# Kernel tuning notes

Hardware: AMD Instinct MI355X
Metric: run time of the kernel (lower is better)

The kernel has to match this reference:

```python
import jax, jax.numpy as jnp
import numpy as np

N_NODES = 512   # hidden_dim in the original code == number of graph nodes
SEQ = 64
DIN = 128
HEADS = 4
DOUT = 128
E = 4096
NEG_SLOPE = 0.2
LN_EPS = 1e-5


def _init(key, shape, fan_in):
    return (jax.random.normal(key, shape, jnp.float32) / np.sqrt(fan_in)).astype(jnp.float32)


def setup_inputs() -> dict:
    key = jax.random.key(0)
    ks = jax.random.split(key, 16)
    x = jax.random.normal(ks[0], (N_NODES, SEQ, DIN), jnp.float32)
    src = jax.random.randint(ks[1], (E,), 0, N_NODES, dtype=jnp.int32)
    # guarantee every node has >=1 incoming edge (DGL requires nonzero in-degree)
    dst = jnp.concatenate([
        jnp.arange(N_NODES, dtype=jnp.int32),
        jax.random.randint(ks[2], (E - N_NODES,), 0, N_NODES, dtype=jnp.int32),
    ])
    return {
        "x": x, "src": src, "dst": dst,
        # GATv2 layer 0: DIN -> DIN, 4 heads (separate fc_src / fc_dst, share_weights=False)
        "W1s": _init(ks[3], (DIN, HEADS * DIN), DIN), "b1s": jnp.zeros((HEADS * DIN,), jnp.float32),
        "W1d": _init(ks[4], (DIN, HEADS * DIN), DIN), "b1d": jnp.zeros((HEADS * DIN,), jnp.float32),
        "attn1": _init(ks[5], (HEADS, DIN), DIN),
        # GATv2 layer 1: DIN*HEADS -> DIN, 1 head
        "W2s": _init(ks[6], (HEADS * DIN, DIN), HEADS * DIN), "b2s": jnp.zeros((DIN,), jnp.float32),
        "W2d": _init(ks[7], (HEADS * DIN, DIN), HEADS * DIN), "b2d": jnp.zeros((DIN,), jnp.float32),
        "attn2": _init(ks[8], (1, DIN), DIN),
        # LayerNorm ln0 + final Linear fc
        "gamma": jnp.ones((DIN,), jnp.float32), "beta": jnp.zeros((DIN,), jnp.float32),
        "Wfc": _init(ks[9], (DIN, DOUT), DIN), "bfc": jnp.zeros((DOUT,), jnp.float32),
    }


def _gatv2(h, src, dst, Ws, bs, Wd, bd, attn, n_nodes, heads, d_out):
    """DGL GATv2Conv: h [N, Din] -> [N, heads, d_out]."""
    fs = (h @ Ws + bs).reshape(-1, heads, d_out)   # [N,H,D]
    fd = (h @ Wd + bd).reshape(-1, heads, d_out)
    e = jax.nn.leaky_relu(fs[src] + fd[dst], NEG_SLOPE)     # [E,H,D]
    logits = jnp.einsum('ehd,hd->eh', e, attn)              # [E,H]
    m = jax.ops.segment_max(logits, dst, num_segments=n_nodes)
    ex = jnp.exp(logits - m[dst])
    den = jax.ops.segment_sum(ex, dst, num_segments=n_nodes)
    alpha = ex / den[dst]                                   # edge softmax per dst node
    return jax.ops.segment_sum(alpha[:, :, None] * fs[src], dst, num_segments=n_nodes)


def reference(x, src, dst, W1s, b1s, W1d, b1d, attn1, W2s, b2s, W2d, b2d, attn2, gamma, beta, Wfc, bfc):
    # preprocess: keep channel 0, log10(rest + 1), NaN -> 0
    xp = jnp.concatenate([x[..., :1], jnp.log10(x[..., 1:] + 1.0)], axis=-1)
    xp = jnp.where(jnp.isnan(xp), 0.0, xp)                  # [N, S, DIN]
    h = jnp.transpose(xp, (1, 0, 2))                        # [S, N, DIN] (seq-batched graph copies)
    g1 = jax.vmap(lambda hh: _gatv2(hh, src, dst, W1s, b1s, W1d, b1d, attn1, N_NODES, HEADS, DIN))(h)
    h2 = g1.reshape(SEQ, N_NODES, HEADS * DIN)              # concat heads
    g2 = jax.vmap(lambda hh: _gatv2(hh, src, dst, W2s, b2s, W2d, b2d, attn2, N_NODES, 1, DIN))(h2)
    g = jnp.transpose(g2[:, :, 0, :], (1, 0, 2))            # [N, S, DIN]
    g = jnp.where(jnp.isnan(g), xp, g)
    out = xp + g                                            # residual; dropout is identity in eval
    mu = jnp.mean(out, axis=-1, keepdims=True)
    var = jnp.mean(jnp.square(out - mu), axis=-1, keepdims=True)
    y = (out - mu) / jnp.sqrt(var + LN_EPS) * gamma + beta  # ln0
    return y @ Wfc + bfc                                    # [N, S, DOUT]
```

## Files before the change

kernel.cpp:

```cpp
#include <hip/hip_runtime.h>
#include <cmath>

#define NN    512
#define SEQL  64
#define DIN   128
#define NH    4
#define NE    4096
#define DOUTN 128

typedef __attribute__((ext_vector_type(4))) float f32x4;
typedef __attribute__((ext_vector_type(8))) short bf16x8;

__device__ __forceinline__ float lrelu(float v) { return v >= 0.f ? v : 0.2f * v; }

__device__ __forceinline__ unsigned short f2bf(float f) {
    union { float f; unsigned u; } x; x.f = f;
    unsigned r = (x.u + 0x7FFFu + ((x.u >> 16) & 1u)) >> 16;
    return (unsigned short)r;
}
__device__ __forceinline__ float bf2f(unsigned short h) {
    union { unsigned u; float f; } x; x.u = ((unsigned)h) << 16;
    return x.f;
}

__global__ __launch_bounds__(256) void preprocess_k(const float* __restrict__ x,
                                                    float* __restrict__ H,
                                                    unsigned short* __restrict__ Hbf) {
    int tid = blockIdx.x * 256 + threadIdx.x;
    int base = tid * 4;
    int d0 = base & 127;
    int s  = (base >> 7) & 63;
    int n  = base >> 13;
    float4 v = *(const float4*)(x + base);
    if (d0 == 0) {
        v.y = log10f(v.y + 1.f); v.z = log10f(v.z + 1.f); v.w = log10f(v.w + 1.f);
    } else {
        v.x = log10f(v.x + 1.f); v.y = log10f(v.y + 1.f);
        v.z = log10f(v.z + 1.f); v.w = log10f(v.w + 1.f);
    }
    if (v.x != v.x) v.x = 0.f;
    if (v.y != v.y) v.y = 0.f;
    if (v.z != v.z) v.z = 0.f;
    if (v.w != v.w) v.w = 0.f;
    size_t off = ((size_t)s * NN + n) * DIN + d0;
    *(float4*)(H + off) = v;
    ushort4 b; b.x = f2bf(v.x); b.y = f2bf(v.y); b.z = f2bf(v.z); b.w = f2bf(v.w);
    *(ushort4*)(Hbf + off) = b;
}

__global__ __launch_bounds__(256) void castw_k(const float* __restrict__ W1s, const float* __restrict__ W1d,
                                               const float* __restrict__ W2s, const float* __restrict__ W2d,
                                               const float* __restrict__ Wfc,
                                               const float* __restrict__ b1s, const float* __restrict__ b1d,
                                               const float* __restrict__ b2s, const float* __restrict__ b2d,
                                               unsigned short* __restrict__ T1sd, unsigned short* __restrict__ T2sd,
                                               unsigned short* __restrict__ Tfc,
                                               float* __restrict__ bc1, float* __restrict__ bc2) {
    int i = blockIdx.x * 256 + threadIdx.x;
    if (i < 131072) {
        int n = i >> 7, k = i & 127;
        T1sd[i] = f2bf(n < 512 ? W1s[k * 512 + n] : W1d[k * 512 + (n - 512)]);
    } else if (i < 262144) {
        int j = i - 131072; int n = j >> 9, k = j & 511;
        T2sd[j] = f2bf(n < 128 ? W2s[k * 128 + n] : W2d[k * 128 + (n - 128)]);
    } else if (i < 278528) {
        int j = i - 262144; int n = j >> 7, k = j & 127;
        Tfc[j] = f2bf(Wfc[k * 128 + n]);
    } else if (i < 279552) {
        int j = i - 278528;
        bc1[j] = j < 512 ? b1s[j] : b1d[j - 512];
    } else if (i < 279808) {
        int j = i - 279552;
        bc2[j] = j < 128 ? b2s[j] : b2d[j - 128];
    }
}

__global__ void csr_init_k(int* counts, int* fill) {
    int t = threadIdx.x;
    counts[t] = 0; fill[t] = 0;
}
__global__ void csr_hist_k(const int* __restrict__ dst, int* counts) {
    int e = blockIdx.x * 256 + threadIdx.x;
    if (e < NE) atomicAdd(&counts[dst[e]], 1);
}
__global__ void csr_scan_k(const int* __restrict__ counts, int* __restrict__ row_ptr) {
    int l = threadIdx.x;
    int c[8]; int lsum = 0;
#pragma unroll
    for (int j = 0; j < 8; ++j) { c[j] = counts[l * 8 + j]; lsum += c[j]; }
    int pre = lsum;
    for (int o = 1; o < 64; o <<= 1) {
        int v = __shfl_up(pre, o);
        if (l >= o) pre += v;
    }
    int acc = pre - lsum;
#pragma unroll
    for (int j = 0; j < 8; ++j) { row_ptr[l * 8 + j] = acc; acc += c[j]; }
    if (l == 63) row_ptr[512] = acc;
}
__global__ void csr_scatter_k(const int* __restrict__ dst, const int* __restrict__ row_ptr,
                              int* fill, int* eidx) {
    int e = blockIdx.x * 256 + threadIdx.x;
    if (e < NE) {
        int dn = dst[e];
        int pos = atomicAdd(&fill[dn], 1);
        eidx[row_ptr[dn] + pos] = e;
    }
}

template<int MODE>
__global__ __launch_bounds__(256) void gemm_k(const unsigned short* __restrict__ A,
                                              const unsigned short* __restrict__ BT,
                                              const float* __restrict__ bias,
                                              void* __restrict__ C1v, void* __restrict__ C2v,
                                              int M, int N, int K, int s0, int half) {
    __shared__ unsigned short As[8192];
    __shared__ unsigned short Bs[8192];
    int t = threadIdx.x;
    int w = t >> 6, l = t & 63;
    int wr = w >> 1, wc = w & 1;
    int m0 = blockIdx.y * 128, n0 = blockIdx.x * 128;

    f32x4 acc[4][4];
#pragma unroll
    for (int i = 0; i < 4; ++i)
#pragma unroll
        for (int j = 0; j < 4; ++j) acc[i][j] = (f32x4){0.f, 0.f, 0.f, 0.f};

    for (int k0 = 0; k0 < K; k0 += 64) {
        bf16x8 ra[4], rb[4];
#pragma unroll
        for (int r = 0; r < 4; ++r) {
            int q = t * 16 + r * 4096;
            int row = q >> 7;
            int cole = (q & 127) >> 1;
            ra[r] = *(const bf16x8*)(A  + (size_t)(m0 + row) * K + k0 + cole);
            rb[r] = *(const bf16x8*)(BT + (size_t)(n0 + row) * K + k0 + cole);
        }
        __syncthreads();
#pragma unroll
        for (int r = 0; r < 4; ++r) {
            int q = t * 16 + r * 4096;
            int row = q >> 7;
            int phys = (row << 7) | ((q & 127) ^ ((row & 7) << 4));
            *(bf16x8*)((char*)As + phys) = ra[r];
            *(bf16x8*)((char*)Bs + phys) = rb[r];
        }
        __syncthreads();
#pragma unroll
        for (int ks = 0; ks < 2; ++ks) {
            bf16x8 af[4], bfr[4];
#pragma unroll
            for (int i = 0; i < 4; ++i) {
                int row = wr * 64 + i * 16 + (l & 15);
                int colb = (ks * 64 + ((l >> 4) * 16)) ^ ((row & 7) << 4);
                af[i] = *(const bf16x8*)((const char*)As + (row << 7) + colb);
            }
#pragma unroll
            for (int j = 0; j < 4; ++j) {
                int row = wc * 64 + j * 16 + (l & 15);
                int colb = (ks * 64 + ((l >> 4) * 16)) ^ ((row & 7) << 4);
                bfr[j] = *(const bf16x8*)((const char*)Bs + (row << 7) + colb);
            }
#pragma unroll
            for (int i = 0; i < 4; ++i)
#pragma unroll
                for (int j = 0; j < 4; ++j)
                    acc[i][j] = __builtin_amdgcn_mfma_f32_16x16x32_bf16(af[i], bfr[j], acc[i][j], 0, 0, 0);
        }
    }

    float bl[4];
#pragma unroll
    for (int j = 0; j < 4; ++j) bl[j] = bias[n0 + wc * 64 + j * 16 + (l & 15)];
#pragma unroll
    for (int i = 0; i < 4; ++i) {
#pragma unroll
        for (int j = 0; j < 4; ++j) {
            int n = n0 + wc * 64 + j * 16 + (l & 15);
#pragma unroll
            for (int jj = 0; jj < 4; ++jj) {
                int m = m0 + wr * 64 + i * 16 + (l >> 4) * 4 + jj;
                float v = acc[i][j][jj] + bl[j];
                if (MODE == 1) {
                    int sl = m >> 9, node = m & 511;
                    ((float*)C1v)[((size_t)node * SEQL + (s0 + sl)) * DOUTN + n] = v;
                } else if (MODE == 2) {
                    unsigned short* dp = (unsigned short*)(n < half ? C1v : C2v);
                    int nn = n < half ? n : n - half;
                    dp[(size_t)m * half + nn] = f2bf(v);
                } else {
                    ((unsigned short*)C1v)[(size_t)m * N + n] = f2bf(v);
                }
            }
        }
    }
}

__device__ __forceinline__ void s_swizzle(int bid, int sc, int B, int logB, int& s, int& idx) {
    if ((sc & 7) == 0) {
        int xcd = bid & 7;
        int j = bid >> 3;
        int grp = j >> logB;
        idx = j & (B - 1);
        s = grp * 8 + xcd;
    } else {
        s = bid >> logB;
        idx = bid & (B - 1);
    }
}

__global__ __launch_bounds__(256) void fused_l1_k(const unsigned short* __restrict__ FS,
                                                  const unsigned short* __restrict__ FD,
                                                  const int* __restrict__ src,
                                                  const int* __restrict__ row_ptr,
                                                  const int* __restrict__ eidx,
                                                  const float* __restrict__ attn,
                                                  unsigned short* __restrict__ G1,
                                                  int sc) {
    int wv = threadIdx.x >> 6, l = threadIdx.x & 63;
    int s, nb;
    s_swizzle(blockIdx.x, sc, 128, 7, s, nb);
    int n = nb * 4 + wv;
    int e0 = row_ptr[n], e1 = row_ptr[n + 1];
    float at[8], fdv[8];
    bf16x8 fdr = *(const bf16x8*)(FD + ((size_t)s * NN + n) * 512 + l * 8);
#pragma unroll
    for (int k = 0; k < 8; ++k) { at[k] = attn[l * 8 + k]; fdv[k] = bf2f((unsigned short)fdr[k]); }
    const unsigned short* fsbase = FS + (size_t)s * NN * 512 + l * 8;
    float m_run = -INFINITY, den = 0.f;
    float acc[8] = {};
    for (int j = e0; j < e1; ++j) {
        int e = eidx[j];
        bf16x8 raw = *(const bf16x8*)(fsbase + (size_t)src[e] * 512);
        float fv[8], part = 0.f;
#pragma unroll
        for (int k = 0; k < 8; ++k) {
            fv[k] = bf2f((unsigned short)raw[k]);
            part += at[k] * lrelu(fv[k] + fdv[k]);
        }
        part += __shfl_xor(part, 1);
        part += __shfl_xor(part, 2);
        part += __shfl_xor(part, 4);
        part += __shfl_xor(part, 8);
        if (part > m_run) {
            float sc_ = expf(m_run - part);
            den = den * sc_ + 1.f;
#pragma unroll
            for (int k = 0; k < 8; ++k) acc[k] = acc[k] * sc_ + fv[k];
            m_run = part;
        } else {
            float w = expf(part - m_run);
            den += w;
#pragma unroll
            for (int k = 0; k < 8; ++k) acc[k] += w * fv[k];
        }
    }
    float inv = 1.f / den;
    bf16x8 o8;
#pragma unroll
    for (int k = 0; k < 8; ++k) o8[k] = (short)f2bf(acc[k] * inv);
    *(bf16x8*)(G1 + ((size_t)s * NN + n) * 512 + l * 8) = o8;
}

__global__ __launch_bounds__(256) void fused_l2_k(const unsigned short* __restrict__ FS,
                                                  const unsigned short* __restrict__ FD,
                                                  const int* __restrict__ src,
                                                  const int* __restrict__ row_ptr,
                                                  const int* __restrict__ eidx,
                                                  const float* __restrict__ attn,
                                                  const float* __restrict__ H,
                                                  const float* __restrict__ gamma,
                                                  const float* __restrict__ beta,
                                                  unsigned short* __restrict__ Y,
                                                  int s0, int sc) {
    int wv = threadIdx.x >> 6, l = threadIdx.x & 63;
    int s, nb;
    s_swizzle(blockIdx.x, sc, 128, 7, s, nb);
    int n = nb * 4 + wv;
    int e0 = row_ptr[n], e1 = row_ptr[n + 1];
    float a0 = attn[l * 2], a1 = attn[l * 2 + 1];
    ushort2 fdr = *(const ushort2*)(FD + ((size_t)s * NN + n) * 128 + l * 2);
    float fd0 = bf2f(fdr.x), fd1 = bf2f(fdr.y);
    const unsigned short* fb = FS + (size_t)s * NN * 128 + l * 2;
    float m_run = -INFINITY, den = 0.f, c0 = 0.f, c1 = 0.f;
    for (int j = e0; j < e1; ++j) {
        int e = eidx[j];
        ushort2 uv = *(const ushort2*)(fb + (size_t)src[e] * 128);
        float f0 = bf2f(uv.x), f1 = bf2f(uv.y);
        float part = a0 * lrelu(f0 + fd0) + a1 * lrelu(f1 + fd1);
#pragma unroll
        for (int o = 1; o < 64; o <<= 1) part += __shfl_xor(part, o);
        if (part > m_run) {
            float sc_ = expf(m_run - part);
            den = den * sc_ + 1.f;
            c0 = c0 * sc_ + f0;
            c1 = c1 * sc_ + f1;
            m_run = part;
        } else {
            float w = expf(part - m_run);
            den += w;
            c0 += w * f0;
            c1 += w * f1;
        }
    }
    float inv = 1.f / den;
    float g0 = c0 * inv, g1 = c1 * inv;
    float2 xp = *(const float2*)(H + ((size_t)(s0 + s) * NN + n) * DIN + l * 2);
    if (g0 != g0) g0 = xp.x;
    if (g1 != g1) g1 = xp.y;
    float o0 = xp.x + g0, o1 = xp.y + g1;
    float ssum = o0 + o1, ssq = o0 * o0 + o1 * o1;
#pragma unroll
    for (int o = 32; o > 0; o >>= 1) { ssum += __shfl_xor(ssum, o); ssq += __shfl_xor(ssq, o); }
    float mu  = ssum * (1.f / 128.f);
    float var = ssq * (1.f / 128.f) - mu * mu;
    float rstd = rsqrtf(var + 1e-5f);
    float y0 = (o0 - mu) * rstd * gamma[l * 2]     + beta[l * 2];
    float y1 = (o1 - mu) * rstd * gamma[l * 2 + 1] + beta[l * 2 + 1];
    ushort2 yo; yo.x = f2bf(y0); yo.y = f2bf(y1);
    *(ushort2*)(Y + ((size_t)s * NN + n) * 128 + l * 2) = yo;
}

extern "C" void kernel_launch(void* const* d_in, const int* in_sizes, int n_in,
                              void* d_out, int out_size, void* d_ws, size_t ws_size,
                              hipStream_t stream) {
    const float* x     = (const float*)d_in[0];
    const int*   src   = (const int*)d_in[1];
    const int*   dst   = (const int*)d_in[2];
    const float* W1s   = (const float*)d_in[3];
    const float* b1s   = (const float*)d_in[4];
    const float* W1d   = (const float*)d_in[5];
    const float* b1d   = (const float*)d_in[6];
    const float* attn1 = (const float*)d_in[7];
    const float* W2s   = (const float*)d_in[8];
    const float* b2s   = (const float*)d_in[9];
    const float* W2d   = (const float*)d_in[10];
    const float* b2d   = (const float*)d_in[11];
    const float* attn2 = (const float*)d_in[12];
    const float* gamma = (const float*)d_in[13];
    const float* beta  = (const float*)d_in[14];
    const float* Wfc   = (const float*)d_in[15];
    const float* bfc   = (const float*)d_in[16];
    float* out = (float*)d_out;

    char* p = (char*)d_ws;
    float*          H    = (float*)p;
    unsigned short* Hbf  = (unsigned short*)(p + 16777216);
    unsigned short* T1sd = (unsigned short*)(p + 25165824);
    unsigned short* T2sd = (unsigned short*)(p + 25427968);
    unsigned short* Tfc  = (unsigned short*)(p + 25690112);
    float*          bc1  = (float*)(p + 25722880);
    float*          bc2  = (float*)(p + 25726976);
    int* counts  = (int*)(p + 25728000);
    int* row_ptr = counts + 512;
    int* fill    = row_ptr + 513;
    int* eidx    = fill + 512;
    const size_t base = 25755648;

    int SC = 1;
    const int cand[7] = {64, 32, 16, 8, 4, 2, 1};
    for (int i = 0; i < 7; ++i)
        if (base + (size_t)cand[i] * 1966080ull <= ws_size) { SC = cand[i]; break; }

    unsigned short* FSb  = (unsigned short*)(p + base);
    unsigned short* FDb  = FSb  + (size_t)SC * 262144;
    unsigned short* G1b  = FDb  + (size_t)SC * 262144;
    unsigned short* FS2b = G1b  + (size_t)SC * 262144;
    unsigned short* FD2b = FS2b + (size_t)SC * 65536;
    unsigned short* Ybf  = FD2b + (size_t)SC * 65536;

    preprocess_k<<<4096, 256, 0, stream>>>(x, H, Hbf);
    castw_k<<<1094, 256, 0, stream>>>(W1s, W1d, W2s, W2d, Wfc, b1s, b1d, b2s, b2d,
                                      T1sd, T2sd, Tfc, bc1, bc2);
    csr_init_k<<<1, 512, 0, stream>>>(counts, fill);
    csr_hist_k<<<NE / 256, 256, 0, stream>>>(dst, counts);
    csr_scan_k<<<1, 64, 0, stream>>>(counts, row_ptr);
    csr_scatter_k<<<NE / 256, 256, 0, stream>>>(dst, row_ptr, fill, eidx);

    for (int s0 = 0; s0 < SEQL; s0 += SC) {
        const unsigned short* Hc = Hbf + (size_t)s0 * NN * DIN;
        int M = SC * NN;
        gemm_k<2><<<dim3(8, SC * 4), 256, 0, stream>>>(Hc, T1sd, bc1, FSb, FDb, M, 1024, 128, 0, 512);
        fused_l1_k<<<SC * 128, 256, 0, stream>>>(FSb, FDb, src, row_ptr, eidx, attn1, G1b, SC);
        gemm_k<2><<<dim3(2, SC * 4), 256, 0, stream>>>(G1b, T2sd, bc2, FS2b, FD2b, M, 256, 512, 0, 128);
        fused_l2_k<<<SC * 128, 256, 0, stream>>>(FS2b, FD2b, src, row_ptr, eidx, attn2,
                                                 H, gamma, beta, Ybf, s0, SC);
        gemm_k<1><<<dim3(1, SC * 4), 256, 0, stream>>>(Ybf, Tfc, bfc, out, nullptr, M, 128, 128, s0, 0);
    }
}
```

Before: 265.9 us.

## Store source ids in CSR, batch gather loads by four, use exp2

The CSR scatter now stores each edge's source node directly, which removes the dependent eidx->src double indirection in both attention kernels. The edge loops in the fused GATv2 kernels issue up to four independent feature gathers before processing them, so more memory loads are in flight per wave. The attention weights are pre-scaled by log2(e) so the online softmax can use exp2f instead of expf. The unrolled loop adds branches for the remainder edges and some register pressure.

```diff
diff --git a/kernel.cpp b/kernel.cpp
--- a/kernel.cpp
+++ b/kernel.cpp
@@ -7,6 +7,7 @@
 #define NH    4
 #define NE    4096
 #define DOUTN 128
+#define LOG2E 1.44269504088896340736f
 
 typedef __attribute__((ext_vector_type(4))) float f32x4;
 typedef __attribute__((ext_vector_type(8))) short bf16x8;
@@ -98,13 +99,13 @@
     for (int j = 0; j < 8; ++j) { row_ptr[l * 8 + j] = acc; acc += c[j]; }
     if (l == 63) row_ptr[512] = acc;
 }
-__global__ void csr_scatter_k(const int* __restrict__ dst, const int* __restrict__ row_ptr,
-                              int* fill, int* eidx) {
+__global__ void csr_scatter_k(const int* __restrict__ src, const int* __restrict__ dst,
+                              const int* __restrict__ row_ptr, int* fill, int* esrc) {
     int e = blockIdx.x * 256 + threadIdx.x;
     if (e < NE) {
         int dn = dst[e];
         int pos = atomicAdd(&fill[dn], 1);
-        eidx[row_ptr[dn] + pos] = e;
+        esrc[row_ptr[dn] + pos] = src[e];
     }
 }
 
@@ -212,9 +213,8 @@
 
 __global__ __launch_bounds__(256) void fused_l1_k(const unsigned short* __restrict__ FS,
                                                   const unsigned short* __restrict__ FD,
-                                                  const int* __restrict__ src,
                                                   const int* __restrict__ row_ptr,
-                                                  const int* __restrict__ eidx,
+                                                  const int* __restrict__ esrc,
                                                   const float* __restrict__ attn,
                                                   unsigned short* __restrict__ G1,
                                                   int sc) {
@@ -226,13 +226,15 @@
     float at[8], fdv[8];
     bf16x8 fdr = *(const bf16x8*)(FD + ((size_t)s * NN + n) * 512 + l * 8);
 #pragma unroll
-    for (int k = 0; k < 8; ++k) { at[k] = attn[l * 8 + k]; fdv[k] = bf2f((unsigned short)fdr[k]); }
+    for (int k = 0; k < 8; ++k) {
+        at[k] = attn[l * 8 + k] * LOG2E;
+        fdv[k] = bf2f((unsigned short)fdr[k]);
+    }
     const unsigned short* fsbase = FS + (size_t)s * NN * 512 + l * 8;
     float m_run = -INFINITY, den = 0.f;
     float acc[8] = {};
-    for (int j = e0; j < e1; ++j) {
-        int e = eidx[j];
-        bf16x8 raw = *(const bf16x8*)(fsbase + (size_t)src[e] * 512);
+
+    auto process = [&](bf16x8 raw) {
         float fv[8], part = 0.f;
 #pragma unroll
         for (int k = 0; k < 8; ++k) {
@@ -244,17 +246,30 @@
         part += __shfl_xor(part, 4);
         part += __shfl_xor(part, 8);
         if (part > m_run) {
-            float sc_ = expf(m_run - part);
+            float sc_ = exp2f(m_run - part);
             den = den * sc_ + 1.f;
 #pragma unroll
             for (int k = 0; k < 8; ++k) acc[k] = acc[k] * sc_ + fv[k];
             m_run = part;
         } else {
-            float w = expf(part - m_run);
+            float w = exp2f(part - m_run);
             den += w;
 #pragma unroll
             for (int k = 0; k < 8; ++k) acc[k] += w * fv[k];
         }
+    };
+
+    for (int j = e0; j < e1; j += 4) {
+        int rem = e1 - j;
+        bf16x8 r0, r1, r2, r3;
+        r0 = *(const bf16x8*)(fsbase + (size_t)esrc[j] * 512);
+        if (rem > 1) r1 = *(const bf16x8*)(fsbase + (size_t)esrc[j + 1] * 512);
+        if (rem > 2) r2 = *(const bf16x8*)(fsbase + (size_t)esrc[j + 2] * 512);
+        if (rem > 3) r3 = *(const bf16x8*)(fsbase + (size_t)esrc[j + 3] * 512);
+        process(r0);
+        if (rem > 1) process(r1);
+        if (rem > 2) process(r2);
+        if (rem > 3) process(r3);
     }
     float inv = 1.f / den;
     bf16x8 o8;
@@ -265,9 +280,8 @@
 
 __global__ __launch_bounds__(256) void fused_l2_k(const unsigned short* __restrict__ FS,
                                                   const unsigned short* __restrict__ FD,
-                                                  const int* __restrict__ src,
                                                   const int* __restrict__ row_ptr,
-                                                  const int* __restrict__ eidx,
+                                                  const int* __restrict__ esrc,
                                                   const float* __restrict__ attn,
                                                   const float* __restrict__ H,
                                                   const float* __restrict__ gamma,
@@ -279,30 +293,42 @@
     s_swizzle(blockIdx.x, sc, 128, 7, s, nb);
     int n = nb * 4 + wv;
     int e0 = row_ptr[n], e1 = row_ptr[n + 1];
-    float a0 = attn[l * 2], a1 = attn[l * 2 + 1];
+    float a0 = attn[l * 2] * LOG2E, a1 = attn[l * 2 + 1] * LOG2E;
     ushort2 fdr = *(const ushort2*)(FD + ((size_t)s * NN + n) * 128 + l * 2);
     float fd0 = bf2f(fdr.x), fd1 = bf2f(fdr.y);
     const unsigned short* fb = FS + (size_t)s * NN * 128 + l * 2;
     float m_run = -INFINITY, den = 0.f, c0 = 0.f, c1 = 0.f;
-    for (int j = e0; j < e1; ++j) {
-        int e = eidx[j];
-        ushort2 uv = *(const ushort2*)(fb + (size_t)src[e] * 128);
+
+    auto process = [&](ushort2 uv) {
         float f0 = bf2f(uv.x), f1 = bf2f(uv.y);
         float part = a0 * lrelu(f0 + fd0) + a1 * lrelu(f1 + fd1);
 #pragma unroll
         for (int o = 1; o < 64; o <<= 1) part += __shfl_xor(part, o);
         if (part > m_run) {
-            float sc_ = expf(m_run - part);
+            float sc_ = exp2f(m_run - part);
             den = den * sc_ + 1.f;
             c0 = c0 * sc_ + f0;
             c1 = c1 * sc_ + f1;
             m_run = part;
         } else {
-            float w = expf(part - m_run);
+            float w = exp2f(part - m_run);
             den += w;
             c0 += w * f0;
             c1 += w * f1;
         }
+    };
+
+    for (int j = e0; j < e1; j += 4) {
+        int rem = e1 - j;
+        ushort2 u0, u1, u2, u3;
+        u0 = *(const ushort2*)(fb + (size_t)esrc[j] * 128);
+        if (rem > 1) u1 = *(const ushort2*)(fb + (size_t)esrc[j + 1] * 128);
+        if (rem > 2) u2 = *(const ushort2*)(fb + (size_t)esrc[j + 2] * 128);
+        if (rem > 3) u3 = *(const ushort2*)(fb + (size_t)esrc[j + 3] * 128);
+        process(u0);
+        if (rem > 1) process(u1);
+        if (rem > 2) process(u2);
+        if (rem > 3) process(u3);
     }
     float inv = 1.f / den;
     float g0 = c0 * inv, g1 = c1 * inv;
@@ -355,7 +381,7 @@
     int* counts  = (int*)(p + 25728000);
     int* row_ptr = counts + 512;
     int* fill    = row_ptr + 513;
-    int* eidx    = fill + 512;
+    int* esrc    = fill + 512;
     const size_t base = 25755648;
 
     int SC = 1;
@@ -376,15 +402,15 @@
     csr_init_k<<<1, 512, 0, stream>>>(counts, fill);
     csr_hist_k<<<NE / 256, 256, 0, stream>>>(dst, counts);
     csr_scan_k<<<1, 64, 0, stream>>>(counts, row_ptr);
-    csr_scatter_k<<<NE / 256, 256, 0, stream>>>(dst, row_ptr, fill, eidx);
+    csr_scatter_k<<<NE / 256, 256, 0, stream>>>(src, dst, row_ptr, fill, esrc);
 
     for (int s0 = 0; s0 < SEQL; s0 += SC) {
         const unsigned short* Hc = Hbf + (size_t)s0 * NN * DIN;
         int M = SC * NN;
         gemm_k<2><<<dim3(8, SC * 4), 256, 0, stream>>>(Hc, T1sd, bc1, FSb, FDb, M, 1024, 128, 0, 512);
-        fused_l1_k<<<SC * 128, 256, 0, stream>>>(FSb, FDb, src, row_ptr, eidx, attn1, G1b, SC);
+        fused_l1_k<<<SC * 128, 256, 0, stream>>>(FSb, FDb, row_ptr, esrc, attn1, G1b, SC);
         gemm_k<2><<<dim3(2, SC * 4), 256, 0, stream>>>(G1b, T2sd, bc2, FS2b, FD2b, M, 256, 512, 0, 128);
-        fused_l2_k<<<SC * 128, 256, 0, stream>>>(FS2b, FD2b, src, row_ptr, eidx, attn2,
+        fused_l2_k<<<SC * 128, 256, 0, stream>>>(FS2b, FD2b, row_ptr, esrc, attn2,
                                                  H, gamma, beta, Ybf, s0, SC);
         gemm_k<1><<<dim3(1, SC * 4), 256, 0, stream>>>(Ybf, Tfc, bfc, out, nullptr, M, 128, 128, s0, 0);
     }
```

Result: faster. 247.9 us (-6.8%).
